# Kernel tuning notes

Measured on AMD Instinct MI355X. Metric: run time of the kernel, lower is better.

Reference implementation:

```python
import jax, jax.numpy as jnp
import numpy as np

E = 32          # n_routed_experts / num_local_experts
H = 1024        # hidden_size
I = 512         # moe_intermediate_size
G = 8           # n_group
TKG = 4         # topk_group
TOPK = 8        # num_experts_per_tok
NSH = 2         # n_shared_experts
SCALE = 2.5     # routed_scaling_factor


def setup_inputs() -> dict:
    key = jax.random.key(0)
    ks = jax.random.split(key, 10)
    s = 0.02
    return {
        "hidden_states": jax.random.normal(ks[0], (2, 1024, H), jnp.float32),
        # router: linear weight [E, H] and e_score_correction_bias [E]
        "gate_w": jax.random.normal(ks[1], (E, H), jnp.float32) * s,
        "gate_bias": jax.random.normal(ks[2], (E,), jnp.float32) * s,
        # routed experts (stacked SwiGLU weights, torch Linear layout [out, in])
        "w_gate": jax.random.normal(ks[3], (E, I, H), jnp.float32) * s,
        "w_up": jax.random.normal(ks[4], (E, I, H), jnp.float32) * s,
        "w_down": jax.random.normal(ks[5], (E, H, I), jnp.float32) * s,
        # shared experts: one MLP with intermediate = I * NSH
        "sh_gate": jax.random.normal(ks[6], (I * NSH, H), jnp.float32) * s,
        "sh_up": jax.random.normal(ks[7], (I * NSH, H), jnp.float32) * s,
        "sh_down": jax.random.normal(ks[8], (H, I * NSH), jnp.float32) * s,
    }


def reference(hidden_states, gate_w, gate_bias, w_gate, w_up, w_down,
              sh_gate, sh_up, sh_down):
    B, S, Hd = hidden_states.shape
    h = hidden_states.reshape(-1, Hd)                      # [T, H]

    # ---- router (DeepseekV3TopkRouter + route_tokens_to_experts) ----
    logits = h.astype(jnp.float32) @ gate_w.T              # [T, E]
    scores = jax.nn.sigmoid(logits)
    sc = scores + gate_bias                                # scores_for_choice
    # group score = sum of top-2 expert scores within each group
    grp = sc.reshape(-1, G, E // G)                        # [T, G, E/G]
    group_scores = jax.lax.top_k(grp, 2)[0].sum(-1)        # [T, G]
    gidx = jax.lax.top_k(group_scores, TKG)[1]             # [T, TKG]
    gmask = jnp.sum(jax.nn.one_hot(gidx, G, dtype=sc.dtype), axis=1)  # [T, G]
    smask = jnp.repeat(gmask, E // G, axis=1)              # [T, E]
    masked = jnp.where(smask > 0, sc, jnp.zeros_like(sc))  # masked_fill(~mask, 0)
    tki = jax.lax.top_k(masked, TOPK)[1]                   # [T, TOPK]
    tkw = jnp.take_along_axis(scores, tki, axis=1)         # gather raw sigmoid scores
    tkw = tkw / (tkw.sum(-1, keepdims=True) + 1e-20)       # norm_topk_prob
    tkw = tkw * SCALE

    # ---- dispatch-compute-combine (experts_forward) ----
    # combine[t, e] = sum_k tkw[t, k] * [tki[t, k] == e]
    combine = (jax.nn.one_hot(tki, E, dtype=tkw.dtype) * tkw[..., None]).sum(1)  # [T, E]
    g = jax.nn.silu(jnp.einsum('th,eih->tei', h, w_gate))  # [T, E, I]
    u = jnp.einsum('th,eih->tei', h, w_up)                 # [T, E, I]
    routed = jnp.einsum('tei,ehi->th', g * u * combine[:, :, None], w_down)  # [T, H]

    # ---- shared experts ----
    sg = jax.nn.silu(h @ sh_gate.T)
    shared = (sg * (h @ sh_up.T)) @ sh_down.T              # [T, H]

    return (routed + shared).reshape(B, S, Hd)
```

## Files before the change

### kernel.cpp

```cpp
#include <hip/hip_runtime.h>
#include <hip/hip_bf16.h>
#include <cstdint>

#define E_ 32
#define H_ 1024
#define I_ 512
#define G_ 8
#define NSH_ 2
#define SCALE_ 2.5f
#define NROUTED (E_ * I_)
#define PADCAP (16384 + E_ * 128)

typedef unsigned short u16;
using bf16x8_t = __attribute__((ext_vector_type(8))) __bf16;
using f32x4_t  = __attribute__((ext_vector_type(4))) float;

__device__ __forceinline__ u16 f2bf(float x) {
  union { float f; uint32_t u; } v; v.f = x;
  uint32_t u = v.u;
  uint32_t r = (u + 0x7fffu + ((u >> 16) & 1u)) >> 16;
  return (u16)r;
}
__device__ __forceinline__ float bf2f(u16 x) {
  union { uint32_t u; float f; } v; v.u = ((uint32_t)x) << 16; return v.f;
}

__device__ __forceinline__ void load_lds16(const void* g, void* l) {
  __builtin_amdgcn_global_load_lds(
      (const __attribute__((address_space(1))) unsigned int*)g,
      (__attribute__((address_space(3))) unsigned int*)l,
      16, 0, 0);
}

#define OFF_BU   16777216L
#define OFF_BD   33554432L
#define OFF_BSHG 50331648L
#define OFF_BSHU 51380224L
#define OFF_BSHD 52428800L
#define WBF_TOT  53477376L

__global__ void init_kernel(const float* __restrict__ gw, float* __restrict__ gwT,
                            int* __restrict__ counts, int* __restrict__ cursor,
                            int* __restrict__ qheads,
                            int* __restrict__ tok_list, float* __restrict__ wt_list) {
  int i = blockIdx.x * blockDim.x + threadIdx.x;
  if (i < H_ * E_) {
    int k = i >> 5, e = i & 31;
    gwT[i] = gw[(long)e * H_ + k];
  }
  if (i < PADCAP) { tok_list[i] = 0; wt_list[i] = 0.f; }
  if (i < E_) { counts[i] = 0; cursor[i] = 0; }
  if (i < 2) qheads[i] = 0;
}

#define W4_WG  4194304L
#define W4_WU  8388608L
#define W4_WD  12582912L
#define W4_SHG 12845056L
#define W4_SHU 13107200L
#define W4_TOT 13369344L
__global__ void cvtw_kernel(const float* __restrict__ wg, const float* __restrict__ wu,
                            const float* __restrict__ wd, const float* __restrict__ shg,
                            const float* __restrict__ shu, const float* __restrict__ shd,
                            u16* __restrict__ wbf) {
  long i = (long)blockIdx.x * blockDim.x + threadIdx.x;
  long stride = (long)gridDim.x * blockDim.x;
  for (; i < W4_TOT; i += stride) {
    const float* s; long off; long dofs;
    if (i < W4_WG)       { s = wg;  off = i;            dofs = off * 4; }
    else if (i < W4_WU)  { s = wu;  off = i - W4_WG;    dofs = OFF_BU + off * 4; }
    else if (i < W4_WD)  { s = wd;  off = i - W4_WU;    dofs = OFF_BD + off * 4; }
    else if (i < W4_SHG) { s = shg; off = i - W4_WD;    dofs = OFF_BSHG + off * 4; }
    else if (i < W4_SHU) { s = shu; off = i - W4_SHG;   dofs = OFF_BSHU + off * 4; }
    else                 { s = shd; off = i - W4_SHU;   dofs = OFF_BSHD + off * 4; }
    float4 v = ((const float4*)s)[off];
    ushort4 o;
    o.x = f2bf(v.x); o.y = f2bf(v.y); o.z = f2bf(v.z); o.w = f2bf(v.w);
    *(ushort4*)(wbf + dofs) = o;
  }
}

__global__ __launch_bounds__(256) void logits_kernel(
    const float* __restrict__ h, const float* __restrict__ gwT,
    float* __restrict__ logits, u16* __restrict__ hbf) {
  __shared__ float sh[8][H_];
  const int tid = threadIdx.x;
  const int t0 = blockIdx.x * 8;
  #pragma unroll
  for (int c = tid; c < 8 * H_ / 4; c += 256) {
    int row = c / (H_ / 4), col = c % (H_ / 4);
    float4 v = ((const float4*)(h + (size_t)(t0 + row) * H_))[col];
    ((float4*)sh[row])[col] = v;
    ushort4 o;
    o.x = f2bf(v.x); o.y = f2bf(v.y); o.z = f2bf(v.z); o.w = f2bf(v.w);
    ((ushort4*)(hbf + (size_t)(t0 + row) * H_))[col] = o;
  }
  __syncthreads();
  const int w = tid >> 6, l = tid & 63;
  const int e = l & 31, tl = w * 2 + (l >> 5);
  const float* hp = sh[tl];
  const float* wp = gwT + e;
  float acc = 0.f;
  #pragma unroll 8
  for (int k = 0; k < H_; ++k) acc += hp[k] * wp[(size_t)k * E_];
  logits[(size_t)(t0 + tl) * E_ + e] = acc;
}

__global__ __launch_bounds__(256) void topk_kernel(
    const float* __restrict__ logits, const float* __restrict__ gb,
    int* __restrict__ idx8, float* __restrict__ wt8, int* __restrict__ counts) {
  __shared__ float s_sc[256][33];
  const int lt = threadIdx.x;
  const int t = blockIdx.x * 256 + lt;
  float sc[E_];
  #pragma unroll
  for (int e = 0; e < E_; ++e) {
    float lg = logits[(size_t)t * E_ + e];
    float sig = 1.f / (1.f + __expf(-lg));
    s_sc[lt][e] = sig;
    sc[e] = sig + gb[e];
  }
  float gs[G_];
  #pragma unroll
  for (int g = 0; g < G_; ++g) {
    float a = sc[g * 4], b = sc[g * 4 + 1], c = sc[g * 4 + 2], d = sc[g * 4 + 3];
    float hi1 = fmaxf(a, b), lo1 = fminf(a, b);
    float hi2 = fmaxf(c, d), lo2 = fminf(c, d);
    float m1 = fmaxf(hi1, hi2);
    float m2 = (hi1 >= hi2) ? fmaxf(lo1, hi2) : fmaxf(lo2, hi1);
    gs[g] = m1 + m2;
  }
  unsigned gm = 0;
  #pragma unroll
  for (int r = 0; r < 4; ++r) {
    float bv = -1e30f; int bi = 0;
    #pragma unroll
    for (int g = 0; g < G_; ++g)
      if (!(gm & (1u << g)) && gs[g] > bv) { bv = gs[g]; bi = g; }
    gm |= 1u << bi;
  }
  float msk[E_];
  #pragma unroll
  for (int e = 0; e < E_; ++e)
    msk[e] = ((gm >> (e >> 2)) & 1u) ? sc[e] : 0.f;
  unsigned um = 0; float wsum = 0.f;
  int idxs[8]; float wts[8];
  #pragma unroll
  for (int r = 0; r < 8; ++r) {
    float bv = -1e30f; int bi = 0;
    #pragma unroll
    for (int e = 0; e < E_; ++e)
      if (!(um & (1u << e)) && msk[e] > bv) { bv = msk[e]; bi = e; }
    um |= 1u << bi;
    idxs[r] = bi;
    float wv = s_sc[lt][bi];
    wts[r] = wv; wsum += wv;
  }
  float inv = SCALE_ / (wsum + 1e-20f);
  #pragma unroll
  for (int r = 0; r < 8; ++r) {
    idx8[(size_t)t * 8 + r] = idxs[r];
    wt8[(size_t)t * 8 + r] = wts[r] * inv;
    atomicAdd(&counts[idxs[r]], 1);
  }
}

__global__ void fill_kernel(const int* __restrict__ idx8, const float* __restrict__ wt8,
                            const int* __restrict__ counts, int* __restrict__ cursor,
                            int* __restrict__ tok_list, float* __restrict__ wt_list,
                            int* __restrict__ pair_pos, int npair) {
  int i = blockIdx.x * blockDim.x + threadIdx.x;
  if (i >= npair) return;
  int e = idx8[i];
  int offz = 0;
  for (int k = 0; k < E_; ++k) {
    if (k == e) break;
    offz += ((counts[k] + 127) >> 7) << 7;
  }
  int p = atomicAdd(&cursor[e], 1);
  int slot = offz + p;
  tok_list[slot] = i >> 3;
  wt_list[slot] = wt8[i];
  pair_pos[i] = slot;
}

__global__ __launch_bounds__(256, 2) void p1_kernel(
    const u16* __restrict__ hbf,
    const u16* __restrict__ wbf,
    const int* __restrict__ counts,
    const int* __restrict__ tok_list, const float* __restrict__ wt_list,
    int* __restrict__ qheads,
    u16* __restrict__ gu,
    u16* __restrict__ gu_sh,
    int T) {
  __shared__ u16 lsA[128 * 64];
  __shared__ u16 lsB0[128 * 64];
  __shared__ u16 lsB1[128 * 64];
  __shared__ int s_tok[128];
  __shared__ float s_wt[128];
  __shared__ int s_off[E_], s_ntt[E_];
  __shared__ int s_tot, s_tile;

  const int tid = threadIdx.x;
  if (tid == 0) {
    int run = 0, tot = 0;
    for (int e = 0; e < E_; ++e) {
      s_off[e] = run;
      int nt = (counts[e] + 127) >> 7;
      s_ntt[e] = nt;
      run += nt << 7;
      tot += nt * 4;
    }
    s_tot = tot + (T / 128) * 8;
  }

  const int w = tid >> 6, l = tid & 63;
  const int wr = w >> 1, wc = w & 1;
  const int lr = l & 15, lh = l >> 4;
  const int sw = lr & 7;

  for (;;) {
    __syncthreads();
    if (tid == 0) s_tile = atomicAdd(&qheads[0], 1);
    __syncthreads();
    int q = s_tile;
    if (q >= s_tot) break;

    int z = 0, rem = q;
    for (; z < E_; ++z) { int t = s_ntt[z] * 4; if (rem < t) break; rem -= t; }
    const bool sh_e = (z == E_);
    int tt, nb;
    if (sh_e) { tt = rem >> 3; nb = rem & 7; }
    else      { tt = rem >> 2; nb = rem & 3; }
    const int off = sh_e ? 0 : s_off[z];

    if (tid < 128) {
      if (sh_e) { s_tok[tid] = tt * 128 + tid; s_wt[tid] = 1.0f; }
      else {
        int slot = off + tt * 128 + tid;
        s_tok[tid] = tok_list[slot];
        s_wt[tid] = wt_list[slot];
      }
    }
    __syncthreads();

    const u16* Bg = sh_e ? (wbf + OFF_BSHG + (size_t)(nb * 128) * H_)
                         : (wbf + ((size_t)z * I_ + nb * 128) * H_);
    const u16* Bu = sh_e ? (wbf + OFF_BSHU + (size_t)(nb * 128) * H_)
                         : (wbf + OFF_BU + ((size_t)z * I_ + nb * 128) * H_);

    f32x4_t acc0[4][4], acc1[4][4];
    #pragma unroll
    for (int m = 0; m < 4; ++m)
      #pragma unroll
      for (int n = 0; n < 4; ++n) {
        acc0[m][n] = (f32x4_t){0.f, 0.f, 0.f, 0.f};
        acc1[m][n] = (f32x4_t){0.f, 0.f, 0.f, 0.f};
      }

    for (int k0 = 0; k0 < H_; k0 += 64) {
      #pragma unroll
      for (int i = 0; i < 4; ++i) {
        int c = tid + 256 * i;
        int row = c >> 3, cb = c & 7;
        int scb = cb ^ (row & 7);
        load_lds16(hbf + (size_t)s_tok[row] * H_ + k0 + scb * 8, (char*)lsA + c * 16);
        load_lds16(Bg + (size_t)row * H_ + k0 + scb * 8, (char*)lsB0 + c * 16);
        load_lds16(Bu + (size_t)row * H_ + k0 + scb * 8, (char*)lsB1 + c * 16);
      }
      __syncthreads();
      #pragma unroll
      for (int kk = 0; kk < 64; kk += 32) {
        const int sb = kk >> 3;
        const int blk = ((sb + lh) ^ sw) << 3;
        bf16x8_t af[4], b0f[4], b1f[4];
        #pragma unroll
        for (int m = 0; m < 4; ++m)
          af[m] = *(const bf16x8_t*)(lsA + (wr * 64 + m * 16 + lr) * 64 + blk);
        #pragma unroll
        for (int n = 0; n < 4; ++n) {
          b0f[n] = *(const bf16x8_t*)(lsB0 + (wc * 64 + n * 16 + lr) * 64 + blk);
          b1f[n] = *(const bf16x8_t*)(lsB1 + (wc * 64 + n * 16 + lr) * 64 + blk);
        }
        #pragma unroll
        for (int m = 0; m < 4; ++m)
          #pragma unroll
          for (int n = 0; n < 4; ++n) {
            acc0[m][n] = __builtin_amdgcn_mfma_f32_16x16x32_bf16(af[m], b0f[n], acc0[m][n], 0, 0, 0);
            acc1[m][n] = __builtin_amdgcn_mfma_f32_16x16x32_bf16(af[m], b1f[n], acc1[m][n], 0, 0, 0);
          }
      }
      __syncthreads();
    }

    const int ldo = sh_e ? (I_ * NSH_) : I_;
    u16* outp = sh_e ? (gu_sh + (size_t)(tt * 128) * ldo + nb * 128)
                     : (gu + (size_t)(off + tt * 128) * ldo + nb * 128);
    #pragma unroll
    for (int m = 0; m < 4; ++m) {
      #pragma unroll
      for (int n = 0; n < 4; ++n) {
        int col = wc * 64 + n * 16 + lr;
        #pragma unroll
        for (int j = 0; j < 4; ++j) {
          int trow = wr * 64 + m * 16 + lh * 4 + j;
          float gv = acc0[m][n][j], uv = acc1[m][n][j];
          float sv = gv / (1.f + __expf(-gv));
          outp[(size_t)trow * ldo + col] = f2bf(sv * uv * s_wt[trow]);
        }
      }
    }
  }
}

__global__ __launch_bounds__(256, 3) void p2_kernel(
    const u16* __restrict__ gu, const u16* __restrict__ gu_sh,
    const u16* __restrict__ wbf,
    const int* __restrict__ counts,
    int* __restrict__ qheads,
    u16* __restrict__ part,
    u16* __restrict__ part_sh,
    int T) {
  __shared__ u16 lsA[128 * 64];
  __shared__ u16 lsB[128 * 64];
  __shared__ int s_off[E_], s_ntt[E_];
  __shared__ int s_tot, s_tile;

  const int tid = threadIdx.x;
  if (tid == 0) {
    int run = 0, tot = 0;
    for (int e = 0; e < E_; ++e) {
      s_off[e] = run;
      int nt = (counts[e] + 127) >> 7;
      s_ntt[e] = nt;
      run += nt << 7;
      tot += nt * 8;
    }
    s_tot = tot + (T / 128) * 8;
  }

  const int w = tid >> 6, l = tid & 63;
  const int wr = w >> 1, wc = w & 1;
  const int lr = l & 15, lh = l >> 4;
  const int sw = lr & 7;

  for (;;) {
    __syncthreads();
    if (tid == 0) s_tile = atomicAdd(&qheads[1], 1);
    __syncthreads();
    int q = s_tile;
    if (q >= s_tot) break;

    int z = 0, rem = q;
    for (; z < E_; ++z) { int t = s_ntt[z] * 8; if (rem < t) break; rem -= t; }
    const bool sh_e = (z == E_);
    int tt = rem >> 3, nb = rem & 7;

    const int K = sh_e ? (I_ * NSH_) : I_;
    const int NT = K / 64;
    const u16* Ab = sh_e ? (gu_sh + (size_t)(tt * 128) * K)
                         : (gu + (size_t)(s_off[z] + tt * 128) * K);
    const u16* Bb = sh_e ? (wbf + OFF_BSHD + (size_t)(nb * 128) * K)
                         : (wbf + OFF_BD + (size_t)z * H_ * I_ + (size_t)(nb * 128) * K);
    u16* outp = sh_e ? (part_sh + (size_t)(tt * 128) * H_ + nb * 128)
                     : (part + (size_t)(s_off[z] + tt * 128) * H_ + nb * 128);

    f32x4_t acc[4][4];
    #pragma unroll
    for (int m = 0; m < 4; ++m)
      #pragma unroll
      for (int n = 0; n < 4; ++n) acc[m][n] = (f32x4_t){0.f, 0.f, 0.f, 0.f};

    for (int s = 0; s < NT; ++s) {
      int k0 = s * 64;
      #pragma unroll
      for (int i = 0; i < 4; ++i) {
        int c = tid + 256 * i;
        int row = c >> 3, cb = c & 7;
        int scb = cb ^ (row & 7);
        load_lds16(Ab + (size_t)row * K + k0 + scb * 8, (char*)lsA + c * 16);
        load_lds16(Bb + (size_t)row * K + k0 + scb * 8, (char*)lsB + c * 16);
      }
      __syncthreads();
      #pragma unroll
      for (int kk = 0; kk < 64; kk += 32) {
        const int sb = kk >> 3;
        const int blk = ((sb + lh) ^ sw) << 3;
        bf16x8_t af[4], bf[4];
        #pragma unroll
        for (int m = 0; m < 4; ++m)
          af[m] = *(const bf16x8_t*)(lsA + (wr * 64 + m * 16 + lr) * 64 + blk);
        #pragma unroll
        for (int n = 0; n < 4; ++n)
          bf[n] = *(const bf16x8_t*)(lsB + (wc * 64 + n * 16 + lr) * 64 + blk);
        #pragma unroll
        for (int m = 0; m < 4; ++m)
          #pragma unroll
          for (int n = 0; n < 4; ++n)
            acc[m][n] = __builtin_amdgcn_mfma_f32_16x16x32_bf16(af[m], bf[n], acc[m][n], 0, 0, 0);
      }
      __syncthreads();
    }

    #pragma unroll
    for (int m = 0; m < 4; ++m) {
      #pragma unroll
      for (int n = 0; n < 4; ++n) {
        int col = wc * 64 + n * 16 + lr;
        #pragma unroll
        for (int j = 0; j < 4; ++j) {
          int trow = wr * 64 + m * 16 + lh * 4 + j;
          outp[(size_t)trow * H_ + col] = f2bf(acc[m][n][j]);
        }
      }
    }
  }
}

__global__ void combine_kernel(const u16* __restrict__ part, const u16* __restrict__ part_sh,
                               const int* __restrict__ pair_pos, float* __restrict__ out) {
  int t = blockIdx.x;
  int h = threadIdx.x * 4;
  int pp[8];
  #pragma unroll
  for (int s = 0; s < 8; ++s) pp[s] = pair_pos[(long)t * 8 + s];
  ushort4 v = *(const ushort4*)(part_sh + (size_t)t * H_ + h);
  float a0 = bf2f(v.x), a1 = bf2f(v.y), a2 = bf2f(v.z), a3 = bf2f(v.w);
  #pragma unroll
  for (int s = 0; s < 8; ++s) {
    ushort4 u = *(const ushort4*)(part + (size_t)pp[s] * H_ + h);
    a0 += bf2f(u.x); a1 += bf2f(u.y); a2 += bf2f(u.z); a3 += bf2f(u.w);
  }
  float4 o = {a0, a1, a2, a3};
  *(float4*)(out + (size_t)t * H_ + h) = o;
}

extern "C" void kernel_launch(void* const* d_in, const int* in_sizes, int n_in,
                              void* d_out, int out_size, void* d_ws, size_t ws_size,
                              hipStream_t stream) {
  const float* hs  = (const float*)d_in[0];
  const float* gw  = (const float*)d_in[1];
  const float* gb  = (const float*)d_in[2];
  const float* wg  = (const float*)d_in[3];
  const float* wu  = (const float*)d_in[4];
  const float* wd  = (const float*)d_in[5];
  const float* shg = (const float*)d_in[6];
  const float* shu = (const float*)d_in[7];
  const float* shd = (const float*)d_in[8];
  float* out = (float*)d_out;

  const int T = in_sizes[0] / H_;

  char* ws = (char*)d_ws;
  size_t off = 0;
  auto alloc = [&](size_t bytes) {
    char* p = ws + off;
    off += (bytes + 255) & ~(size_t)255;
    return p;
  };
  int*   counts   = (int*)alloc(E_ * 4);
  int*   cursor   = (int*)alloc(E_ * 4);
  int*   qheads   = (int*)alloc(2 * 4);
  int*   idx8     = (int*)alloc((size_t)T * 8 * 4);
  float* wt8      = (float*)alloc((size_t)T * 8 * 4);
  int*   pair_pos = (int*)alloc((size_t)T * 8 * 4);
  int*   tok_list = (int*)alloc(PADCAP * 4);
  float* wt_list  = (float*)alloc(PADCAP * 4);
  float* gwT      = (float*)alloc((size_t)H_ * E_ * 4);
  float* logits   = (float*)alloc((size_t)T * E_ * 4);
  u16* hbf     = (u16*)alloc((size_t)T * H_ * 2);
  u16* wbf     = (u16*)alloc((size_t)WBF_TOT * 2);
  u16* gu      = (u16*)alloc((size_t)PADCAP * I_ * 2);
  u16* gu_sh   = (u16*)alloc((size_t)T * I_ * NSH_ * 2);
  u16* part    = (u16*)alloc((size_t)PADCAP * H_ * 2);
  u16* part_sh = (u16*)alloc((size_t)T * H_ * 2);
  if (off > ws_size) return;

  hipLaunchKernelGGL(init_kernel, dim3(128), dim3(256), 0, stream,
                     gw, gwT, counts, cursor, qheads, tok_list, wt_list);

  hipLaunchKernelGGL(logits_kernel, dim3(T / 8), dim3(256), 0, stream,
                     hs, gwT, logits, hbf);
  hipLaunchKernelGGL(topk_kernel, dim3(T / 256), dim3(256), 0, stream,
                     logits, gb, idx8, wt8, counts);
  hipLaunchKernelGGL(fill_kernel, dim3((T * 8 + 255) / 256), dim3(256), 0, stream,
                     idx8, wt8, counts, cursor, tok_list, wt_list, pair_pos, T * 8);

  hipLaunchKernelGGL(cvtw_kernel, dim3(4096), dim3(256), 0, stream,
                     wg, wu, wd, shg, shu, shd, wbf);

  hipLaunchKernelGGL(p1_kernel, dim3(512), dim3(256), 0, stream,
                     hbf, wbf, counts, tok_list, wt_list, qheads, gu, gu_sh, T);

  hipLaunchKernelGGL(p2_kernel, dim3(768), dim3(256), 0, stream,
                     gu, gu_sh, wbf, counts, qheads, part, part_sh, T);

  hipLaunchKernelGGL(combine_kernel, dim3(T), dim3(256), 0, stream,
                     part, part_sh, pair_pos, out);
}
```

Baseline: 326.5 us.

## Double-buffer GEMM LDS tiles and fuse init/convert and logits/topk kernels

The p1 and p2 GEMM loops move from single-buffered 64-wide K tiles to double-buffered 32-wide tiles, issuing the next stage's global-to-LDS loads before computing the current one. This overlaps memory latency with MFMA work, and the LDS swizzle is reworked to suit the narrower tile. The init and weight-conversion kernels are merged into one prep kernel, and the logits and top-k kernels into one router kernel, cutting launches and the logits round-trip through global memory. In the fused router only 8 threads per block run the top-k step, which serialises that part of the work.

```diff
diff --git a/kernel.cpp b/kernel.cpp
--- a/kernel.cpp
+++ b/kernel.cpp
@@ -39,33 +39,31 @@
 #define OFF_BSHD 52428800L
 #define WBF_TOT  53477376L
 
-__global__ void init_kernel(const float* __restrict__ gw, float* __restrict__ gwT,
-                            int* __restrict__ counts, int* __restrict__ cursor,
-                            int* __restrict__ qheads,
-                            int* __restrict__ tok_list, float* __restrict__ wt_list) {
-  int i = blockIdx.x * blockDim.x + threadIdx.x;
-  if (i < H_ * E_) {
-    int k = i >> 5, e = i & 31;
-    gwT[i] = gw[(long)e * H_ + k];
-  }
-  if (i < PADCAP) { tok_list[i] = 0; wt_list[i] = 0.f; }
-  if (i < E_) { counts[i] = 0; cursor[i] = 0; }
-  if (i < 2) qheads[i] = 0;
-}
-
 #define W4_WG  4194304L
 #define W4_WU  8388608L
 #define W4_WD  12582912L
 #define W4_SHG 12845056L
 #define W4_SHU 13107200L
 #define W4_TOT 13369344L
-__global__ void cvtw_kernel(const float* __restrict__ wg, const float* __restrict__ wu,
+__global__ void prep_kernel(const float* __restrict__ gw, float* __restrict__ gwT,
+                            int* __restrict__ counts, int* __restrict__ cursor,
+                            int* __restrict__ qheads,
+                            int* __restrict__ tok_list, float* __restrict__ wt_list,
+                            const float* __restrict__ wg, const float* __restrict__ wu,
                             const float* __restrict__ wd, const float* __restrict__ shg,
                             const float* __restrict__ shu, const float* __restrict__ shd,
                             u16* __restrict__ wbf) {
-  long i = (long)blockIdx.x * blockDim.x + threadIdx.x;
+  long i0 = (long)blockIdx.x * blockDim.x + threadIdx.x;
+  if (i0 < H_ * E_) {
+    int k = (int)(i0 >> 5), e = (int)(i0 & 31);
+    gwT[i0] = gw[(long)e * H_ + k];
+  }
+  if (i0 < PADCAP) { tok_list[i0] = 0; wt_list[i0] = 0.f; }
+  if (i0 < E_) { counts[i0] = 0; cursor[i0] = 0; }
+  if (i0 < 2) qheads[i0] = 0;
+
   long stride = (long)gridDim.x * blockDim.x;
-  for (; i < W4_TOT; i += stride) {
+  for (long i = i0; i < W4_TOT; i += stride) {
     const float* s; long off; long dofs;
     if (i < W4_WG)       { s = wg;  off = i;            dofs = off * 4; }
     else if (i < W4_WU)  { s = wu;  off = i - W4_WG;    dofs = OFF_BU + off * 4; }
@@ -80,10 +78,12 @@
   }
 }
 
-__global__ __launch_bounds__(256) void logits_kernel(
+__global__ __launch_bounds__(256) void router_kernel(
     const float* __restrict__ h, const float* __restrict__ gwT,
-    float* __restrict__ logits, u16* __restrict__ hbf) {
+    const float* __restrict__ gb, u16* __restrict__ hbf,
+    int* __restrict__ idx8, float* __restrict__ wt8, int* __restrict__ counts) {
   __shared__ float sh[8][H_];
+  __shared__ float s_log[8][E_ + 1];
   const int tid = threadIdx.x;
   const int t0 = blockIdx.x * 8;
   #pragma unroll
@@ -96,72 +96,69 @@
     ((ushort4*)(hbf + (size_t)(t0 + row) * H_))[col] = o;
   }
   __syncthreads();
-  const int w = tid >> 6, l = tid & 63;
-  const int e = l & 31, tl = w * 2 + (l >> 5);
-  const float* hp = sh[tl];
-  const float* wp = gwT + e;
-  float acc = 0.f;
-  #pragma unroll 8
-  for (int k = 0; k < H_; ++k) acc += hp[k] * wp[(size_t)k * E_];
-  logits[(size_t)(t0 + tl) * E_ + e] = acc;
-}
-
-__global__ __launch_bounds__(256) void topk_kernel(
-    const float* __restrict__ logits, const float* __restrict__ gb,
-    int* __restrict__ idx8, float* __restrict__ wt8, int* __restrict__ counts) {
-  __shared__ float s_sc[256][33];
-  const int lt = threadIdx.x;
-  const int t = blockIdx.x * 256 + lt;
-  float sc[E_];
-  #pragma unroll
-  for (int e = 0; e < E_; ++e) {
-    float lg = logits[(size_t)t * E_ + e];
-    float sig = 1.f / (1.f + __expf(-lg));
-    s_sc[lt][e] = sig;
-    sc[e] = sig + gb[e];
-  }
-  float gs[G_];
-  #pragma unroll
-  for (int g = 0; g < G_; ++g) {
-    float a = sc[g * 4], b = sc[g * 4 + 1], c = sc[g * 4 + 2], d = sc[g * 4 + 3];
-    float hi1 = fmaxf(a, b), lo1 = fminf(a, b);
-    float hi2 = fmaxf(c, d), lo2 = fminf(c, d);
-    float m1 = fmaxf(hi1, hi2);
-    float m2 = (hi1 >= hi2) ? fmaxf(lo1, hi2) : fmaxf(lo2, hi1);
-    gs[g] = m1 + m2;
-  }
-  unsigned gm = 0;
-  #pragma unroll
-  for (int r = 0; r < 4; ++r) {
-    float bv = -1e30f; int bi = 0;
-    #pragma unroll
-    for (int g = 0; g < G_; ++g)
-      if (!(gm & (1u << g)) && gs[g] > bv) { bv = gs[g]; bi = g; }
-    gm |= 1u << bi;
-  }
-  float msk[E_];
-  #pragma unroll
-  for (int e = 0; e < E_; ++e)
-    msk[e] = ((gm >> (e >> 2)) & 1u) ? sc[e] : 0.f;
-  unsigned um = 0; float wsum = 0.f;
-  int idxs[8]; float wts[8];
-  #pragma unroll
-  for (int r = 0; r < 8; ++r) {
-    float bv = -1e30f; int bi = 0;
+  {
+    const int w = tid >> 6, l = tid & 63;
+    const int e = l & 31, tl = w * 2 + (l >> 5);
+    const float* hp = sh[tl];
+    const float* wp = gwT + e;
+    float acc = 0.f;
+    #pragma unroll 8
+    for (int k = 0; k < H_; ++k) acc += hp[k] * wp[(size_t)k * E_];
+    s_log[tl][e] = acc;
+  }
+  __syncthreads();
+  if (tid < 8) {
+    const int t = t0 + tid;
+    float scr[E_], sc[E_];
+    #pragma unroll
+    for (int e = 0; e < E_; ++e) {
+      float sig = 1.f / (1.f + __expf(-s_log[tid][e]));
+      scr[e] = sig;
+      sc[e] = sig + gb[e];
+    }
+    float gs[G_];
+    #pragma unroll
+    for (int g = 0; g < G_; ++g) {
+      float a = sc[g * 4], b = sc[g * 4 + 1], c = sc[g * 4 + 2], d = sc[g * 4 + 3];
+      float hi1 = fmaxf(a, b), lo1 = fminf(a, b);
+      float hi2 = fmaxf(c, d), lo2 = fminf(c, d);
+      float m1 = fmaxf(hi1, hi2);
+      float m2 = (hi1 >= hi2) ? fmaxf(lo1, hi2) : fmaxf(lo2, hi1);
+      gs[g] = m1 + m2;
+    }
+    unsigned gm = 0;
+    #pragma unroll
+    for (int r = 0; r < 4; ++r) {
+      float bv = -1e30f; int bi = 0;
+      #pragma unroll
+      for (int g = 0; g < G_; ++g)
+        if (!(gm & (1u << g)) && gs[g] > bv) { bv = gs[g]; bi = g; }
+      gm |= 1u << bi;
+    }
+    float msk[E_];
     #pragma unroll
     for (int e = 0; e < E_; ++e)
-      if (!(um & (1u << e)) && msk[e] > bv) { bv = msk[e]; bi = e; }
-    um |= 1u << bi;
-    idxs[r] = bi;
-    float wv = s_sc[lt][bi];
-    wts[r] = wv; wsum += wv;
-  }
-  float inv = SCALE_ / (wsum + 1e-20f);
-  #pragma unroll
-  for (int r = 0; r < 8; ++r) {
-    idx8[(size_t)t * 8 + r] = idxs[r];
-    wt8[(size_t)t * 8 + r] = wts[r] * inv;
-    atomicAdd(&counts[idxs[r]], 1);
+      msk[e] = ((gm >> (e >> 2)) & 1u) ? sc[e] : 0.f;
+    unsigned um = 0; float wsum = 0.f;
+    int idxs[8]; float wts[8];
+    #pragma unroll
+    for (int r = 0; r < 8; ++r) {
+      float bv = -1e30f; int bi = 0;
+      #pragma unroll
+      for (int e = 0; e < E_; ++e)
+        if (!(um & (1u << e)) && msk[e] > bv) { bv = msk[e]; bi = e; }
+      um |= 1u << bi;
+      idxs[r] = bi;
+      float wv = scr[bi];
+      wts[r] = wv; wsum += wv;
+    }
+    float inv = SCALE_ / (wsum + 1e-20f);
+    #pragma unroll
+    for (int r = 0; r < 8; ++r) {
+      idx8[(size_t)t * 8 + r] = idxs[r];
+      wt8[(size_t)t * 8 + r] = wts[r] * inv;
+      atomicAdd(&counts[idxs[r]], 1);
+    }
   }
 }
 
@@ -193,9 +190,9 @@
     u16* __restrict__ gu,
     u16* __restrict__ gu_sh,
     int T) {
-  __shared__ u16 lsA[128 * 64];
-  __shared__ u16 lsB0[128 * 64];
-  __shared__ u16 lsB1[128 * 64];
+  __shared__ u16 lsA[2][128 * 32];
+  __shared__ u16 lsB0[2][128 * 32];
+  __shared__ u16 lsB1[2][128 * 32];
   __shared__ int s_tok[128];
   __shared__ float s_wt[128];
   __shared__ int s_off[E_], s_ntt[E_];
@@ -217,7 +214,11 @@
   const int w = tid >> 6, l = tid & 63;
   const int wr = w >> 1, wc = w & 1;
   const int lr = l & 15, lh = l >> 4;
-  const int sw = lr & 7;
+  const int rdblk = (lh ^ ((lr >> 1) & 3)) << 3;
+
+  const int c0 = tid, c1 = tid + 256;
+  const int row0 = c0 >> 2, cb0 = c0 & 3, scb0 = cb0 ^ ((row0 >> 1) & 3);
+  const int row1 = c1 >> 2, cb1 = c1 & 3, scb1 = cb1 ^ ((row1 >> 1) & 3);
 
   for (;;) {
     __syncthreads();
@@ -248,6 +249,8 @@
                          : (wbf + ((size_t)z * I_ + nb * 128) * H_);
     const u16* Bu = sh_e ? (wbf + OFF_BSHU + (size_t)(nb * 128) * H_)
                          : (wbf + OFF_BU + ((size_t)z * I_ + nb * 128) * H_);
+    const u16* A0 = hbf + (size_t)s_tok[row0] * H_ + scb0 * 8;
+    const u16* A1 = hbf + (size_t)s_tok[row1] * H_ + scb1 * 8;
 
     f32x4_t acc0[4][4], acc1[4][4];
     #pragma unroll
@@ -258,39 +261,42 @@
         acc1[m][n] = (f32x4_t){0.f, 0.f, 0.f, 0.f};
       }
 
-    for (int k0 = 0; k0 < H_; k0 += 64) {
-      #pragma unroll
-      for (int i = 0; i < 4; ++i) {
-        int c = tid + 256 * i;
-        int row = c >> 3, cb = c & 7;
-        int scb = cb ^ (row & 7);
-        load_lds16(hbf + (size_t)s_tok[row] * H_ + k0 + scb * 8, (char*)lsA + c * 16);
-        load_lds16(Bg + (size_t)row * H_ + k0 + scb * 8, (char*)lsB0 + c * 16);
-        load_lds16(Bu + (size_t)row * H_ + k0 + scb * 8, (char*)lsB1 + c * 16);
+    auto stage = [&](int b, int k0) {
+      load_lds16(A0 + k0, (char*)&lsA[b][0] + c0 * 16);
+      load_lds16(A1 + k0, (char*)&lsA[b][0] + c1 * 16);
+      load_lds16(Bg + (size_t)row0 * H_ + k0 + scb0 * 8, (char*)&lsB0[b][0] + c0 * 16);
+      load_lds16(Bg + (size_t)row1 * H_ + k0 + scb1 * 8, (char*)&lsB0[b][0] + c1 * 16);
+      load_lds16(Bu + (size_t)row0 * H_ + k0 + scb0 * 8, (char*)&lsB1[b][0] + c0 * 16);
+      load_lds16(Bu + (size_t)row1 * H_ + k0 + scb1 * 8, (char*)&lsB1[b][0] + c1 * 16);
+    };
+    auto compute = [&](int b) {
+      bf16x8_t af[4], b0f[4], b1f[4];
+      #pragma unroll
+      for (int m = 0; m < 4; ++m)
+        af[m] = *(const bf16x8_t*)(&lsA[b][0] + (wr * 64 + m * 16 + lr) * 32 + rdblk);
+      #pragma unroll
+      for (int n = 0; n < 4; ++n) {
+        b0f[n] = *(const bf16x8_t*)(&lsB0[b][0] + (wc * 64 + n * 16 + lr) * 32 + rdblk);
+        b1f[n] = *(const bf16x8_t*)(&lsB1[b][0] + (wc * 64 + n * 16 + lr) * 32 + rdblk);
       }
-      __syncthreads();
-      #pragma unroll
-      for (int kk = 0; kk < 64; kk += 32) {
-        const int sb = kk >> 3;
-        const int blk = ((sb + lh) ^ sw) << 3;
-        bf16x8_t af[4], b0f[4], b1f[4];
-        #pragma unroll
-        for (int m = 0; m < 4; ++m)
-          af[m] = *(const bf16x8_t*)(lsA + (wr * 64 + m * 16 + lr) * 64 + blk);
+      #pragma unroll
+      for (int m = 0; m < 4; ++m)
         #pragma unroll
         for (int n = 0; n < 4; ++n) {
-          b0f[n] = *(const bf16x8_t*)(lsB0 + (wc * 64 + n * 16 + lr) * 64 + blk);
-          b1f[n] = *(const bf16x8_t*)(lsB1 + (wc * 64 + n * 16 + lr) * 64 + blk);
+          acc0[m][n] = __builtin_amdgcn_mfma_f32_16x16x32_bf16(af[m], b0f[n], acc0[m][n], 0, 0, 0);
+          acc1[m][n] = __builtin_amdgcn_mfma_f32_16x16x32_bf16(af[m], b1f[n], acc1[m][n], 0, 0, 0);
         }
-        #pragma unroll
-        for (int m = 0; m < 4; ++m)
-          #pragma unroll
-          for (int n = 0; n < 4; ++n) {
-            acc0[m][n] = __builtin_amdgcn_mfma_f32_16x16x32_bf16(af[m], b0f[n], acc0[m][n], 0, 0, 0);
-            acc1[m][n] = __builtin_amdgcn_mfma_f32_16x16x32_bf16(af[m], b1f[n], acc1[m][n], 0, 0, 0);
-          }
-      }
+    };
+
+    stage(0, 0);
+    __syncthreads();
+    int cur = 0;
+    #pragma unroll 1
+    for (int s = 0; s < 32; ++s) {
+      if (s < 31) stage(cur ^ 1, (s + 1) * 32);
+      compute(cur);
       __syncthreads();
+      cur ^= 1;
     }
 
     const int ldo = sh_e ? (I_ * NSH_) : I_;
@@ -321,8 +327,8 @@
     u16* __restrict__ part,
     u16* __restrict__ part_sh,
     int T) {
-  __shared__ u16 lsA[128 * 64];
-  __shared__ u16 lsB[128 * 64];
+  __shared__ u16 lsA[2][128 * 32];
+  __shared__ u16 lsB[2][128 * 32];
   __shared__ int s_off[E_], s_ntt[E_];
   __shared__ int s_tot, s_tile;
 
@@ -342,7 +348,11 @@
   const int w = tid >> 6, l = tid & 63;
   const int wr = w >> 1, wc = w & 1;
   const int lr = l & 15, lh = l >> 4;
-  const int sw = lr & 7;
+  const int rdblk = (lh ^ ((lr >> 1) & 3)) << 3;
+
+  const int c0 = tid, c1 = tid + 256;
+  const int row0 = c0 >> 2, cb0 = c0 & 3, scb0 = cb0 ^ ((row0 >> 1) & 3);
+  const int row1 = c1 >> 2, cb1 = c1 & 3, scb1 = cb1 ^ ((row1 >> 1) & 3);
 
   for (;;) {
     __syncthreads();
@@ -357,7 +367,7 @@
     int tt = rem >> 3, nb = rem & 7;
 
     const int K = sh_e ? (I_ * NSH_) : I_;
-    const int NT = K / 64;
+    const int NT = K / 32;
     const u16* Ab = sh_e ? (gu_sh + (size_t)(tt * 128) * K)
                          : (gu + (size_t)(s_off[z] + tt * 128) * K);
     const u16* Bb = sh_e ? (wbf + OFF_BSHD + (size_t)(nb * 128) * K)
@@ -371,35 +381,36 @@
       #pragma unroll
       for (int n = 0; n < 4; ++n) acc[m][n] = (f32x4_t){0.f, 0.f, 0.f, 0.f};
 
-    for (int s = 0; s < NT; ++s) {
-      int k0 = s * 64;
-      #pragma unroll
-      for (int i = 0; i < 4; ++i) {
-        int c = tid + 256 * i;
-        int row = c >> 3, cb = c & 7;
-        int scb = cb ^ (row & 7);
-        load_lds16(Ab + (size_t)row * K + k0 + scb * 8, (char*)lsA + c * 16);
-        load_lds16(Bb + (size_t)row * K + k0 + scb * 8, (char*)lsB + c * 16);
-      }
-      __syncthreads();
-      #pragma unroll
-      for (int kk = 0; kk < 64; kk += 32) {
-        const int sb = kk >> 3;
-        const int blk = ((sb + lh) ^ sw) << 3;
-        bf16x8_t af[4], bf[4];
-        #pragma unroll
-        for (int m = 0; m < 4; ++m)
-          af[m] = *(const bf16x8_t*)(lsA + (wr * 64 + m * 16 + lr) * 64 + blk);
+    auto stage = [&](int b, int k0) {
+      load_lds16(Ab + (size_t)row0 * K + k0 + scb0 * 8, (char*)&lsA[b][0] + c0 * 16);
+      load_lds16(Ab + (size_t)row1 * K + k0 + scb1 * 8, (char*)&lsA[b][0] + c1 * 16);
+      load_lds16(Bb + (size_t)row0 * K + k0 + scb0 * 8, (char*)&lsB[b][0] + c0 * 16);
+      load_lds16(Bb + (size_t)row1 * K + k0 + scb1 * 8, (char*)&lsB[b][0] + c1 * 16);
+    };
+    auto compute = [&](int b) {
+      bf16x8_t af[4], bf[4];
+      #pragma unroll
+      for (int m = 0; m < 4; ++m)
+        af[m] = *(const bf16x8_t*)(&lsA[b][0] + (wr * 64 + m * 16 + lr) * 32 + rdblk);
+      #pragma unroll
+      for (int n = 0; n < 4; ++n)
+        bf[n] = *(const bf16x8_t*)(&lsB[b][0] + (wc * 64 + n * 16 + lr) * 32 + rdblk);
+      #pragma unroll
+      for (int m = 0; m < 4; ++m)
         #pragma unroll
         for (int n = 0; n < 4; ++n)
-          bf[n] = *(const bf16x8_t*)(lsB + (wc * 64 + n * 16 + lr) * 64 + blk);
-        #pragma unroll
-        for (int m = 0; m < 4; ++m)
-          #pragma unroll
-          for (int n = 0; n < 4; ++n)
-            acc[m][n] = __builtin_amdgcn_mfma_f32_16x16x32_bf16(af[m], bf[n], acc[m][n], 0, 0, 0);
-      }
+          acc[m][n] = __builtin_amdgcn_mfma_f32_16x16x32_bf16(af[m], bf[n], acc[m][n], 0, 0, 0);
+    };
+
+    stage(0, 0);
+    __syncthreads();
+    int cur = 0;
+    #pragma unroll 1
+    for (int s = 0; s < NT; ++s) {
+      if (s < NT - 1) stage(cur ^ 1, (s + 1) * 32);
+      compute(cur);
       __syncthreads();
+      cur ^= 1;
     }
 
     #pragma unroll
@@ -467,7 +478,6 @@
   int*   tok_list = (int*)alloc(PADCAP * 4);
   float* wt_list  = (float*)alloc(PADCAP * 4);
   float* gwT      = (float*)alloc((size_t)H_ * E_ * 4);
-  float* logits   = (float*)alloc((size_t)T * E_ * 4);
   u16* hbf     = (u16*)alloc((size_t)T * H_ * 2);
   u16* wbf     = (u16*)alloc((size_t)WBF_TOT * 2);
   u16* gu      = (u16*)alloc((size_t)PADCAP * I_ * 2);
@@ -476,19 +486,16 @@
   u16* part_sh = (u16*)alloc((size_t)T * H_ * 2);
   if (off > ws_size) return;
 
-  hipLaunchKernelGGL(init_kernel, dim3(128), dim3(256), 0, stream,
-                     gw, gwT, counts, cursor, qheads, tok_list, wt_list);
-
-  hipLaunchKernelGGL(logits_kernel, dim3(T / 8), dim3(256), 0, stream,
-                     hs, gwT, logits, hbf);
-  hipLaunchKernelGGL(topk_kernel, dim3(T / 256), dim3(256), 0, stream,
-                     logits, gb, idx8, wt8, counts);
+  hipLaunchKernelGGL(prep_kernel, dim3(4096), dim3(256), 0, stream,
+                     gw, gwT, counts, cursor, qheads, tok_list, wt_list,
+                     wg, wu, wd, shg, shu, shd, wbf);
+
+  hipLaunchKernelGGL(router_kernel, dim3(T / 8), dim3(256), 0, stream,
+                     hs, gwT, gb, hbf, idx8, wt8, counts);
+
   hipLaunchKernelGGL(fill_kernel, dim3((T * 8 + 255) / 256), dim3(256), 0, stream,
                      idx8, wt8, counts, cursor, tok_list, wt_list, pair_pos, T * 8);
 
-  hipLaunchKernelGGL(cvtw_kernel, dim3(4096), dim3(256), 0, stream,
-                     wg, wu, wd, shg, shu, shd, wbf);
-
   hipLaunchKernelGGL(p1_kernel, dim3(512), dim3(256), 0, stream,
                      hbf, wbf, counts, tok_list, wt_list, qheads, gu, gu_sh, T);
 
```

Result: faster. 309.2 us (-5.3%).
